# Kernel optimization log

Measured on AMD Instinct MI355X. Metric: run time of the kernel, lower is better.

## Reference

```python
import jax, jax.numpy as jnp
import numpy as np

D_MODEL = 768
N_HEADS = 12
D_FF = 3072
B, T = 1, 4096
EPS = 1e-5


def _linear_params(key, d_in, d_out):
    kw, kb = jax.random.split(key)
    s = 1.0 / np.sqrt(d_in)
    W = jax.random.uniform(kw, (d_in, d_out), jnp.float32, -s, s)
    b = jax.random.uniform(kb, (d_out,), jnp.float32, -s, s)
    return W, b


def setup_inputs() -> dict:
    key = jax.random.key(0)
    keys = jax.random.split(key, 8)
    x = jax.random.normal(keys[0], (B, T, D_MODEL), jnp.float32)
    Wq, bq = _linear_params(keys[1], D_MODEL, D_MODEL)
    Wk, bk = _linear_params(keys[2], D_MODEL, D_MODEL)
    Wv, bv = _linear_params(keys[3], D_MODEL, D_MODEL)
    Wo, bo = _linear_params(keys[4], D_MODEL, D_MODEL)
    W1, b1 = _linear_params(keys[5], D_MODEL, D_FF)
    W2, b2 = _linear_params(keys[6], D_FF, D_MODEL)
    g1 = jnp.ones((D_MODEL,), jnp.float32)
    be1 = jnp.zeros((D_MODEL,), jnp.float32)
    g2 = jnp.ones((D_MODEL,), jnp.float32)
    be2 = jnp.zeros((D_MODEL,), jnp.float32)
    return {"x": x, "Wq": Wq, "bq": bq, "Wk": Wk, "bk": bk, "Wv": Wv, "bv": bv,
            "Wo": Wo, "bo": bo, "W1": W1, "b1": b1, "W2": W2, "b2": b2,
            "g1": g1, "be1": be1, "g2": g2, "be2": be2}


def _layer_norm(x, g, b):
    mu = jnp.mean(x, axis=-1, keepdims=True)
    var = jnp.var(x, axis=-1, keepdims=True)
    return (x - mu) * jax.lax.rsqrt(var + EPS) * g + b


def reference(x, Wq, bq, Wk, bk, Wv, bv, Wo, bo, W1, b1, W2, b2, g1, be1, g2, be2):
    b_, t_, d_ = x.shape
    dk = d_ // N_HEADS
    # QKV projections -> [B, H, T, dk]
    def split_heads(y):
        return y.reshape(b_, t_, N_HEADS, dk).transpose(0, 2, 1, 3)
    q = split_heads(x @ Wq + bq)
    k = split_heads(x @ Wk + bk)
    v = split_heads(x @ Wv + bv)
    # scores [B, H, T, T], causal mask, softmax
    scores = jnp.einsum('bhqd,bhkd->bhqk', q, k) / np.sqrt(dk).astype(np.float32)
    causal = jnp.tril(jnp.ones((t_, t_), dtype=bool))
    scores = jnp.where(causal, scores, -jnp.inf)
    attn = jax.nn.softmax(scores, axis=-1)
    out = jnp.einsum('bhqk,bhkd->bhqd', attn, v)
    out = out.transpose(0, 2, 1, 3).reshape(b_, t_, d_)
    attn_out = out @ Wo + bo
    # residual + LN1
    h = _layer_norm(x + attn_out, g1, be1)
    # FFN
    ff = jax.nn.relu(h @ W1 + b1) @ W2 + b2
    # residual + LN2
    return _layer_norm(h + ff, g2, be2)
```

## Files before the change

### kernel.cpp

```cpp
#include <hip/hip_runtime.h>
#include <math.h>

#define TSEQ 4096
#define DMODEL 768
#define NHEADS 12
#define DKH 64
#define DFF 3072
#define LOG2E 1.44269504f

typedef __attribute__((ext_vector_type(4))) float f32x4;
typedef __attribute__((ext_vector_type(8))) short s16x8;
typedef unsigned short u16;
typedef unsigned int u32;

__device__ __forceinline__ u16 f2bf(float x) {
    u32 u = __builtin_bit_cast(u32, x);
    u32 r = u + 0x7FFFu + ((u >> 16) & 1u);
    return (u16)(r >> 16);
}
__device__ __forceinline__ float bf2f(u16 h) {
    u32 u = ((u32)h) << 16;
    return __builtin_bit_cast(float, u);
}

__device__ __forceinline__ void gll16(const void* g, void* lds) {
    __builtin_amdgcn_global_load_lds(
        (const __attribute__((address_space(1))) u32*)g,
        (__attribute__((address_space(3))) u32*)lds, 16, 0, 0);
}

__global__ __launch_bounds__(256) void tobf16(const float* __restrict__ in,
                                              u16* __restrict__ out, int n4)
{
    int idx = blockIdx.x * 256 + threadIdx.x;
    for (int i = idx; i < n4; i += 262144) {
        float4 v = *(const float4*)(in + (size_t)i * 4);
        *(ushort4*)(out + (size_t)i * 4) =
            make_ushort4(f2bf(v.x), f2bf(v.y), f2bf(v.z), f2bf(v.w));
    }
}

__global__ __launch_bounds__(256) void wtrans4(
    const float* __restrict__ Wq, const float* __restrict__ Wk,
    const float* __restrict__ Wv, const float* __restrict__ Wo,
    u16* __restrict__ Wqkvt, u16* __restrict__ Wot)
{
    __shared__ float t[32 * 33];
    const int z = blockIdx.z;
    const float* W = (z == 0) ? Wq : (z == 1) ? Wk : (z == 2) ? Wv : Wo;
    u16* out = (z < 3) ? Wqkvt : Wot;
    const int nofs = (z < 3) ? z * 768 : 0;
    const int K = 768, N = 768;
    const int tid = threadIdx.x;
    const int kt = blockIdx.y << 5, nt = blockIdx.x << 5;
    const int r = tid >> 3, c4 = tid & 7;
    float4 v = *(const float4*)(W + (size_t)(kt + r) * N + nt + (c4 << 2));
    t[r * 33 + (c4 << 2) + 0] = v.x;
    t[r * 33 + (c4 << 2) + 1] = v.y;
    t[r * 33 + (c4 << 2) + 2] = v.z;
    t[r * 33 + (c4 << 2) + 3] = v.w;
    __syncthreads();
    float a0 = t[((c4 << 2) + 0) * 33 + r];
    float a1 = t[((c4 << 2) + 1) * 33 + r];
    float a2 = t[((c4 << 2) + 2) * 33 + r];
    float a3 = t[((c4 << 2) + 3) * 33 + r];
    u16* o = out + (size_t)(nofs + nt + r) * K + kt + (c4 << 2);
    *(ushort4*)o = make_ushort4(f2bf(a0), f2bf(a1), f2bf(a2), f2bf(a3));
}

__global__ __launch_bounds__(256) void wtrans(const float* __restrict__ W,
                                              u16* __restrict__ out,
                                              int K, int N)
{
    __shared__ float t[32 * 33];
    const int tid = threadIdx.x;
    const int kt = blockIdx.y << 5, nt = blockIdx.x << 5;
    const int r = tid >> 3, c4 = tid & 7;
    float4 v = *(const float4*)(W + (size_t)(kt + r) * N + nt + (c4 << 2));
    t[r * 33 + (c4 << 2) + 0] = v.x;
    t[r * 33 + (c4 << 2) + 1] = v.y;
    t[r * 33 + (c4 << 2) + 2] = v.z;
    t[r * 33 + (c4 << 2) + 3] = v.w;
    __syncthreads();
    float a0 = t[((c4 << 2) + 0) * 33 + r];
    float a1 = t[((c4 << 2) + 1) * 33 + r];
    float a2 = t[((c4 << 2) + 2) * 33 + r];
    float a3 = t[((c4 << 2) + 3) * 33 + r];
    u16* o = out + (size_t)(nt + r) * K + kt + (c4 << 2);
    *(ushort4*)o = make_ushort4(f2bf(a0), f2bf(a1), f2bf(a2), f2bf(a3));
}

__global__ __launch_bounds__(256) void bias_cat_kernel(const float* bq, const float* bk,
                                                       const float* bv, float* o)
{
    int i = blockIdx.x * 256 + threadIdx.x;
    if (i < 768) o[i] = bq[i];
    else if (i < 1536) o[i] = bk[i - 768];
    else if (i < 2304) o[i] = bv[i - 1536];
}

template<int BM, int BN, int EPI>
__global__ __launch_bounds__(256) void gemm_bf(
    const u16* __restrict__ A, const u16* __restrict__ B,
    const float* __restrict__ bias, const float* __restrict__ R,
    float* __restrict__ Cf, u16* __restrict__ Cs,
    u16* __restrict__ Qb, u16* __restrict__ Kb, u16* __restrict__ VTb,
    int N, int KP)
{
    constexpr int FM = BM / 32, FN = BN / 32, NC = BN / 2, NCP = NC + 4;
    __shared__ u16 As[BM * 64];
    __shared__ u16 Bs[BN * 64];
    __shared__ float Ep[4 * 16 * NCP];

    const int tid = threadIdx.x;
    const int w = tid >> 6, lane = tid & 63;
    const int wr = w >> 1, wc = w & 1;
    const int li = lane & 15, g = lane >> 4;

    const int gX = gridDim.x;
    const int nwg = gridDim.x * gridDim.y;
    const int wid = blockIdx.y * gX + blockIdx.x;
    const int qc = nwg >> 3;
    const int nid = (wid & 7) * qc + (wid >> 3);
    const int m0 = (nid / gX) * BM, n0 = (nid % gX) * BN;

    f32x4 acc[FM][FN];
#pragma unroll
    for (int mi = 0; mi < FM; ++mi)
#pragma unroll
        for (int ni = 0; ni < FN; ++ni) acc[mi][ni] = (f32x4){0.f, 0.f, 0.f, 0.f};

    const int row8 = lane >> 3;
    const int cs = (lane & 7) ^ row8;
    const int l7 = li & 7;

    for (int k0 = 0; k0 < KP; k0 += 64) {
        __syncthreads();
#pragma unroll
        for (int i = 0; i < BM / 32; ++i) {
            int inst = w * (BM / 32) + i;
            const u16* gp = A + (size_t)(m0 + inst * 8 + row8) * KP + k0 + cs * 8;
            gll16(gp, &As[inst * 512]);
        }
#pragma unroll
        for (int i = 0; i < BN / 32; ++i) {
            int inst = w * (BN / 32) + i;
            const u16* gp = B + (size_t)(n0 + inst * 8 + row8) * KP + k0 + cs * 8;
            gll16(gp, &Bs[inst * 512]);
        }
        __syncthreads();
        s16x8 af[FM][2], bfr[FN][2];
#pragma unroll
        for (int mi = 0; mi < FM; ++mi) {
            int Ra = wr * (BM / 2) + mi * 16 + li;
#pragma unroll
            for (int dc = 0; dc < 2; ++dc)
                af[mi][dc] = *(const s16x8*)&As[Ra * 64 + ((dc * 4 + g) ^ l7) * 8];
        }
#pragma unroll
        for (int ni = 0; ni < FN; ++ni) {
            int Rb = wc * (BN / 2) + ni * 16 + li;
#pragma unroll
            for (int dc = 0; dc < 2; ++dc)
                bfr[ni][dc] = *(const s16x8*)&Bs[Rb * 64 + ((dc * 4 + g) ^ l7) * 8];
        }
        __builtin_amdgcn_s_setprio(1);
#pragma unroll
        for (int mi = 0; mi < FM; ++mi)
#pragma unroll
            for (int ni = 0; ni < FN; ++ni) {
                acc[mi][ni] = __builtin_amdgcn_mfma_f32_16x16x32_bf16(
                    af[mi][0], bfr[ni][0], acc[mi][ni], 0, 0, 0);
                acc[mi][ni] = __builtin_amdgcn_mfma_f32_16x16x32_bf16(
                    af[mi][1], bfr[ni][1], acc[mi][ni], 0, 0, 0);
            }
        __builtin_amdgcn_s_setprio(0);
    }
    __syncthreads();

    float* ep = Ep + w * 16 * NCP;
    const int colbase = n0 + wc * NC;
    const int rr = lane >> 2, ch = lane & 3;

#pragma unroll
    for (int mi = 0; mi < FM; ++mi) {
#pragma unroll
        for (int ni = 0; ni < FN; ++ni)
#pragma unroll
            for (int r = 0; r < 4; ++r)
                ep[(g * 4 + r) * NCP + ni * 16 + li] = acc[mi][ni][r];
        asm volatile("s_waitcnt lgkmcnt(0)" ::: "memory");

        const int grow0 = m0 + wr * (BM / 2) + mi * 16;
        const int grow = grow0 + rr;

        if constexpr (EPI == 1) {
#pragma unroll
            for (int q = 0; q < NC / 16; ++q) {
                int col = ch * (NC / 4) + q * 4;
                f32x4 v = *(f32x4*)&ep[rr * NCP + col];
                int gn = colbase + col;
                float4 bb = *(const float4*)(bias + gn);
                float4 rv = *(const float4*)(R + (size_t)grow * N + gn);
                float4 ov;
                ov.x = v[0] + bb.x + rv.x; ov.y = v[1] + bb.y + rv.y;
                ov.z = v[2] + bb.z + rv.z; ov.w = v[3] + bb.w + rv.w;
                *(float4*)(Cf + (size_t)grow * N + gn) = ov;
            }
        } else if constexpr (EPI == 2) {
#pragma unroll
            for (int q = 0; q < NC / 16; ++q) {
                int col = ch * (NC / 4) + q * 4;
                f32x4 v = *(f32x4*)&ep[rr * NCP + col];
                int gn = colbase + col;
                float4 bb = *(const float4*)(bias + gn);
                float x0 = fmaxf(v[0] + bb.x, 0.f), x1 = fmaxf(v[1] + bb.y, 0.f);
                float x2 = fmaxf(v[2] + bb.z, 0.f), x3 = fmaxf(v[3] + bb.w, 0.f);
                *(ushort4*)(Cs + (size_t)grow * N + gn) =
                    make_ushort4(f2bf(x0), f2bf(x1), f2bf(x2), f2bf(x3));
            }
        } else {
            const int seg = colbase / 768;
            const int hh = (colbase % 768) >> 6;
            if (seg < 2) {
                u16* dst = (seg == 0) ? Qb : Kb;
                const float sc2 = (seg == 0) ? 0.125f * LOG2E : 1.0f;
#pragma unroll
                for (int q = 0; q < NC / 16; ++q) {
                    int col = ch * (NC / 4) + q * 4;
                    f32x4 v = *(f32x4*)&ep[rr * NCP + col];
                    float4 bb = *(const float4*)(bias + colbase + col);
                    u16 h0 = f2bf((v[0] + bb.x) * sc2);
                    u16 h1 = f2bf((v[1] + bb.y) * sc2);
                    u16 h2 = f2bf((v[2] + bb.z) * sc2);
                    u16 h3 = f2bf((v[3] + bb.w) * sc2);
                    *(ushort4*)&dst[((size_t)(hh << 12) + grow) * 64 + col] =
                        make_ushort4(h0, h1, h2, h3);
                }
            } else {
                float bb = bias[colbase + lane];
                s16x8 pa, pb;
#pragma unroll
                for (int r2 = 0; r2 < 8; ++r2)
                    pa[r2] = (short)f2bf(ep[r2 * NCP + lane] + bb);
#pragma unroll
                for (int r2 = 0; r2 < 8; ++r2)
                    pb[r2] = (short)f2bf(ep[(8 + r2) * NCP + lane] + bb);
                u16* ov = VTb + ((size_t)(hh << 6) + lane) * TSEQ + grow0;
                *(s16x8*)(ov)     = pa;
                *(s16x8*)(ov + 8) = pb;
            }
        }
    }
}

__global__ __launch_bounds__(256) void attn64(
    const u16* __restrict__ Qb, const u16* __restrict__ Kb,
    const u16* __restrict__ VTb, u16* __restrict__ ctxb)
{
    __shared__ u16 Ks[2][4096];
    __shared__ u16 Vs[2][4096];
    __shared__ u16 Ps[4][1024];

    const int tid = threadIdx.x, w = tid >> 6, lane = tid & 63;
    const int g = lane >> 4, li = lane & 15, l7 = lane & 7;
    const int p = blockIdx.x;
    const int h = blockIdx.y;

    const u16* Qh = Qb + ((size_t)h << 18);
    const u16* Kh = Kb + ((size_t)h << 18);
    const u16* Vh = VTb + ((size_t)h << 18);

    const int row8 = lane >> 3;
    const int cs = (lane & 7) ^ row8;

    for (int pass = 0; pass < 2; ++pass) {
        const int qbk = pass ? 63 - p : p;
        const int q0 = qbk << 6;
        const int nkb = qbk + 1;

        s16x8 qf[2];
#pragma unroll
        for (int dc = 0; dc < 2; ++dc)
            qf[dc] = *(const s16x8*)(Qh + (size_t)(q0 + w * 16 + li) * 64 + dc * 32 + g * 8);

        f32x4 o[4];
        float m_ = -1e30f, l_ = 0.f;
#pragma unroll
        for (int d16 = 0; d16 < 4; ++d16) o[d16] = (f32x4){0.f, 0.f, 0.f, 0.f};

#pragma unroll
        for (int i = 0; i < 2; ++i) {
            int inst = w * 2 + i;
            int row = inst * 8 + row8;
            gll16(Kh + (size_t)row * 64 + cs * 8, &Ks[0][inst * 512]);
            gll16(Vh + (size_t)row * TSEQ + cs * 8, &Vs[0][inst * 512]);
        }
        __syncthreads();

        for (int kb = 0; kb < nkb; ++kb) {
            const int cur = kb & 1;
            if (kb + 1 < nkb) {
                const int kn = kb + 1;
#pragma unroll
                for (int i = 0; i < 2; ++i) {
                    int inst = w * 2 + i;
                    int row = inst * 8 + row8;
                    gll16(Kh + (size_t)((kn << 6) + row) * 64 + cs * 8, &Ks[cur ^ 1][inst * 512]);
                    gll16(Vh + (size_t)row * TSEQ + (kn << 6) + cs * 8, &Vs[cur ^ 1][inst * 512]);
                }
            }

            f32x4 s[4];
            __builtin_amdgcn_s_setprio(1);
#pragma unroll
            for (int c = 0; c < 4; ++c) {
                s[c] = (f32x4){0.f, 0.f, 0.f, 0.f};
                s16x8 a0 = *(const s16x8*)&Ks[cur][(c * 16 + li) * 64 + ((g) ^ l7) * 8];
                s16x8 a1 = *(const s16x8*)&Ks[cur][(c * 16 + li) * 64 + ((4 + g) ^ l7) * 8];
                s[c] = __builtin_amdgcn_mfma_f32_16x16x32_bf16(a0, qf[0], s[c], 0, 0, 0);
                s[c] = __builtin_amdgcn_mfma_f32_16x16x32_bf16(a1, qf[1], s[c], 0, 0, 0);
            }
            __builtin_amdgcn_s_setprio(0);

            if (kb == qbk) {
#pragma unroll
                for (int c = 0; c < 4; ++c)
#pragma unroll
                    for (int r = 0; r < 4; ++r) {
                        int kglob = (kb << 6) + c * 16 + g * 4 + r;
                        int qglob = q0 + w * 16 + li;
                        if (kglob > qglob) s[c][r] = -1e30f;
                    }
            }

            float v0 = fmaxf(fmaxf(s[0][0], s[0][1]), fmaxf(s[0][2], s[0][3]));
            float v1 = fmaxf(fmaxf(s[1][0], s[1][1]), fmaxf(s[1][2], s[1][3]));
            float v2 = fmaxf(fmaxf(s[2][0], s[2][1]), fmaxf(s[2][2], s[2][3]));
            float v3 = fmaxf(fmaxf(s[3][0], s[3][1]), fmaxf(s[3][2], s[3][3]));
            float pm = fmaxf(fmaxf(v0, v1), fmaxf(v2, v3));
            pm = fmaxf(pm, __shfl_xor(pm, 16, 64));
            pm = fmaxf(pm, __shfl_xor(pm, 32, 64));

            int ok = (pm <= m_ + 8.f);
            if (!__all(ok)) {
                float mn = fmaxf(m_, pm);
                float sc2 = exp2f(m_ - mn);
                m_ = mn;
                l_ *= sc2;
#pragma unroll
                for (int r = 0; r < 4; ++r) {
                    float os = __shfl(sc2, g * 4 + r, 64);
#pragma unroll
                    for (int d16 = 0; d16 < 4; ++d16) o[d16][r] *= os;
                }
            }

            float rsum = 0.f;
#pragma unroll
            for (int c = 0; c < 4; ++c) {
                float e0 = exp2f(s[c][0] - m_);
                float e1 = exp2f(s[c][1] - m_);
                float e2 = exp2f(s[c][2] - m_);
                float e3 = exp2f(s[c][3] - m_);
                rsum += (e0 + e1) + (e2 + e3);
                *(ushort4*)&Ps[w][li * 64 + ((c * 16 + 4 * g) ^ (l7 << 3))] =
                    make_ushort4(f2bf(e0), f2bf(e1), f2bf(e2), f2bf(e3));
            }
            rsum += __shfl_xor(rsum, 16, 64);
            rsum += __shfl_xor(rsum, 32, 64);
            l_ += rsum;

            asm volatile("s_waitcnt lgkmcnt(0)" ::: "memory");
            __builtin_amdgcn_sched_barrier(0);

            __builtin_amdgcn_s_setprio(1);
#pragma unroll
            for (int ks = 0; ks < 2; ++ks) {
                int koff = ((ks * 4 + g) ^ l7) * 8;
                s16x8 pf = *(const s16x8*)&Ps[w][li * 64 + ((ks * 32 + g * 8) ^ (l7 << 3))];
#pragma unroll
                for (int d16 = 0; d16 < 4; ++d16) {
                    s16x8 vf = *(const s16x8*)&Vs[cur][(d16 * 16 + li) * 64 + koff];
                    o[d16] = __builtin_amdgcn_mfma_f32_16x16x32_bf16(pf, vf, o[d16], 0, 0, 0);
                }
            }
            __builtin_amdgcn_s_setprio(0);
            __syncthreads();
        }

        float il = 1.0f / l_;
#pragma unroll
        for (int r = 0; r < 4; ++r) {
            float iv = __shfl(il, g * 4 + r, 64);
            int qrow = q0 + w * 16 + g * 4 + r;
#pragma unroll
            for (int d16 = 0; d16 < 4; ++d16) {
                int col = (h << 6) + d16 * 16 + li;
                ctxb[(size_t)qrow * DMODEL + col] = f2bf(o[d16][r] * iv);
            }
        }
        __syncthreads();
    }
}

template<int BF>
__global__ __launch_bounds__(256) void ln_kernel(const float* __restrict__ in,
    const float* __restrict__ gw, const float* __restrict__ bw,
    float* __restrict__ outf, u16* __restrict__ outb)
{
    __shared__ float red[8];
    const int row = blockIdx.x, tid = threadIdx.x;
    const float* x = in + (size_t)row * DMODEL;
    float v0 = x[tid], v1 = x[tid + 256], v2 = x[tid + 512];
    float s = v0 + v1 + v2;
#pragma unroll
    for (int off = 32; off > 0; off >>= 1) s += __shfl_xor(s, off, 64);
    const int wv = tid >> 6, lane = tid & 63;
    if (lane == 0) red[wv] = s;
    __syncthreads();
    float mu = (red[0] + red[1] + red[2] + red[3]) * (1.0f / DMODEL);
    float d0 = v0 - mu, d1 = v1 - mu, d2 = v2 - mu;
    float s2 = d0 * d0 + d1 * d1 + d2 * d2;
#pragma unroll
    for (int off = 32; off > 0; off >>= 1) s2 += __shfl_xor(s2, off, 64);
    if (lane == 0) red[4 + wv] = s2;
    __syncthreads();
    float var = (red[4] + red[5] + red[6] + red[7]) * (1.0f / DMODEL);
    float rstd = rsqrtf(var + 1e-5f);
    float y0 = d0 * rstd * gw[tid] + bw[tid];
    float y1 = d1 * rstd * gw[tid + 256] + bw[tid + 256];
    float y2 = d2 * rstd * gw[tid + 512] + bw[tid + 512];
    float* yo = outf + (size_t)row * DMODEL;
    yo[tid] = y0; yo[tid + 256] = y1; yo[tid + 512] = y2;
    if constexpr (BF) {
        u16* o = outb + (size_t)row * DMODEL;
        o[tid] = f2bf(y0); o[tid + 256] = f2bf(y1); o[tid + 512] = f2bf(y2);
    }
}

extern "C" void kernel_launch(void* const* d_in, const int* in_sizes, int n_in,
                              void* d_out, int out_size, void* d_ws, size_t ws_size,
                              hipStream_t stream)
{
    const float* x  = (const float*)d_in[0];
    const float* Wq = (const float*)d_in[1];  const float* bq = (const float*)d_in[2];
    const float* Wk = (const float*)d_in[3];  const float* bk = (const float*)d_in[4];
    const float* Wv = (const float*)d_in[5];  const float* bv = (const float*)d_in[6];
    const float* Wo = (const float*)d_in[7];  const float* bo = (const float*)d_in[8];
    const float* W1 = (const float*)d_in[9];  const float* b1 = (const float*)d_in[10];
    const float* W2 = (const float*)d_in[11]; const float* b2 = (const float*)d_in[12];
    const float* g1 = (const float*)d_in[13]; const float* be1 = (const float*)d_in[14];
    const float* g2 = (const float*)d_in[15]; const float* be2 = (const float*)d_in[16];
    float* out = (float*)d_out;

    char* wsb = (char*)d_ws;
    u16*   xb    = (u16*)(wsb + 0);
    u16*   Wqkvt = (u16*)(wsb + 6291456);
    u16*   Wot   = (u16*)(wsb + 9830400);
    u16*   W1t   = (u16*)(wsb + 11010048);
    u16*   W2t   = (u16*)(wsb + 15728640);
    float* bcat  = (float*)(wsb + 20447232);
    u16*   Qb    = (u16*)(wsb + 20456448);
    u16*   Kb2   = (u16*)(wsb + 26747904);
    u16*   VTb   = (u16*)(wsb + 33039360);
    u16*   ctxb  = (u16*)(wsb + 39330816);
    float* s1    = (float*)(wsb + 45622272);
    float* h     = (float*)(wsb + 58205184);
    u16*   hb    = (u16*)(wsb + 70788096);
    u16*   ff1b  = (u16*)(wsb + 77079552);
    float* t2    = (float*)(wsb + 102245376);

    tobf16<<<1024, 256, 0, stream>>>(x, xb, 786432);
    wtrans4<<<dim3(24, 24, 4), 256, 0, stream>>>(Wq, Wk, Wv, Wo, Wqkvt, Wot);
    wtrans<<<dim3(96, 24), 256, 0, stream>>>(W1, W1t, 768, 3072);
    wtrans<<<dim3(24, 96), 256, 0, stream>>>(W2, W2t, 3072, 768);
    bias_cat_kernel<<<9, 256, 0, stream>>>(bq, bk, bv, bcat);

    gemm_bf<128, 128, 0><<<dim3(18, 32), 256, 0, stream>>>(
        xb, Wqkvt, bcat, nullptr, nullptr, nullptr, Qb, Kb2, VTb, 2304, 768);
    attn64<<<dim3(32, 12), 256, 0, stream>>>(Qb, Kb2, VTb, ctxb);
    gemm_bf<64, 128, 1><<<dim3(6, 64), 256, 0, stream>>>(
        ctxb, Wot, bo, x, s1, nullptr, nullptr, nullptr, nullptr, 768, 768);
    ln_kernel<1><<<4096, 256, 0, stream>>>(s1, g1, be1, h, hb);
    gemm_bf<128, 128, 2><<<dim3(24, 32), 256, 0, stream>>>(
        hb, W1t, b1, nullptr, nullptr, ff1b, nullptr, nullptr, nullptr, 3072, 768);
    gemm_bf<64, 128, 1><<<dim3(6, 64), 256, 0, stream>>>(
        ff1b, W2t, b2, h, t2, nullptr, nullptr, nullptr, nullptr, 768, 3072);
    ln_kernel<0><<<4096, 256, 0, stream>>>(t2, g2, be2, out, nullptr);
}
```

Measured before the change: 386.1 us.

## Tune attention kernel: XCD-aware block remap, deferred row-sum reduction, packed bf16 convert

The attention grid is flattened to 1D, and block IDs are remapped so that consecutive blocks on the same XCD share a head, which should improve L2 reuse of K/V. The per-iteration cross-lane reductions of the row sum are moved to after the loop, and the max reduction now only runs when a rescale is needed. The checks now use per-lane partial maxima. Float-to-bf16 conversion of probabilities uses the hardware v_cvt_pk_bf16_f32 instruction instead of manual rounding. Load address arithmetic is hoisted into base pointers.

```diff
diff --git a/kernel.cpp b/kernel.cpp
--- a/kernel.cpp
+++ b/kernel.cpp
@@ -21,6 +21,11 @@
 __device__ __forceinline__ float bf2f(u16 h) {
     u32 u = ((u32)h) << 16;
     return __builtin_bit_cast(float, u);
+}
+__device__ __forceinline__ u32 cvtpk(float lo, float hi) {
+    u32 r;
+    asm("v_cvt_pk_bf16_f32 %0, %1, %2" : "=v"(r) : "v"(lo), "v"(hi));
+    return r;
 }
 
 __device__ __forceinline__ void gll16(const void* g, void* lds) {
@@ -264,8 +269,10 @@
 
     const int tid = threadIdx.x, w = tid >> 6, lane = tid & 63;
     const int g = lane >> 4, li = lane & 15, l7 = lane & 7;
-    const int p = blockIdx.x;
-    const int h = blockIdx.y;
+    const int wid = blockIdx.x;
+    const int nid = (wid & 7) * 48 + (wid >> 3);
+    const int h = nid >> 5;
+    const int p = nid & 31;
 
     const u16* Qh = Qb + ((size_t)h << 18);
     const u16* Kh = Kb + ((size_t)h << 18);
@@ -284,6 +291,9 @@
         for (int dc = 0; dc < 2; ++dc)
             qf[dc] = *(const s16x8*)(Qh + (size_t)(q0 + w * 16 + li) * 64 + dc * 32 + g * 8);
 
+        const u16* kbase = Kh + (size_t)(w * 16 + row8) * 64 + cs * 8;
+        const u16* vbase = Vh + (size_t)(w * 16 + row8) * TSEQ + cs * 8;
+
         f32x4 o[4];
         float m_ = -1e30f, l_ = 0.f;
 #pragma unroll
@@ -292,9 +302,8 @@
 #pragma unroll
         for (int i = 0; i < 2; ++i) {
             int inst = w * 2 + i;
-            int row = inst * 8 + row8;
-            gll16(Kh + (size_t)row * 64 + cs * 8, &Ks[0][inst * 512]);
-            gll16(Vh + (size_t)row * TSEQ + cs * 8, &Vs[0][inst * 512]);
+            gll16(kbase + (size_t)i * 512, &Ks[0][inst * 512]);
+            gll16(vbase + (size_t)i * 8 * TSEQ, &Vs[0][inst * 512]);
         }
         __syncthreads();
 
@@ -305,9 +314,8 @@
 #pragma unroll
                 for (int i = 0; i < 2; ++i) {
                     int inst = w * 2 + i;
-                    int row = inst * 8 + row8;
-                    gll16(Kh + (size_t)((kn << 6) + row) * 64 + cs * 8, &Ks[cur ^ 1][inst * 512]);
-                    gll16(Vh + (size_t)row * TSEQ + (kn << 6) + cs * 8, &Vs[cur ^ 1][inst * 512]);
+                    gll16(kbase + (size_t)kn * 4096 + (size_t)i * 512, &Ks[cur ^ 1][inst * 512]);
+                    gll16(vbase + (size_t)kn * 64 + (size_t)i * 8 * TSEQ, &Vs[cur ^ 1][inst * 512]);
                 }
             }
 
@@ -338,12 +346,11 @@
             float v1 = fmaxf(fmaxf(s[1][0], s[1][1]), fmaxf(s[1][2], s[1][3]));
             float v2 = fmaxf(fmaxf(s[2][0], s[2][1]), fmaxf(s[2][2], s[2][3]));
             float v3 = fmaxf(fmaxf(s[3][0], s[3][1]), fmaxf(s[3][2], s[3][3]));
-            float pm = fmaxf(fmaxf(v0, v1), fmaxf(v2, v3));
-            pm = fmaxf(pm, __shfl_xor(pm, 16, 64));
-            pm = fmaxf(pm, __shfl_xor(pm, 32, 64));
-
-            int ok = (pm <= m_ + 8.f);
-            if (!__all(ok)) {
+            float pmp = fmaxf(fmaxf(v0, v1), fmaxf(v2, v3));
+
+            if (!__all(pmp <= m_ + 8.f)) {
+                float pm = fmaxf(pmp, __shfl_xor(pmp, 16, 64));
+                pm = fmaxf(pm, __shfl_xor(pm, 32, 64));
                 float mn = fmaxf(m_, pm);
                 float sc2 = exp2f(m_ - mn);
                 m_ = mn;
@@ -356,20 +363,18 @@
                 }
             }
 
-            float rsum = 0.f;
 #pragma unroll
             for (int c = 0; c < 4; ++c) {
                 float e0 = exp2f(s[c][0] - m_);
                 float e1 = exp2f(s[c][1] - m_);
                 float e2 = exp2f(s[c][2] - m_);
                 float e3 = exp2f(s[c][3] - m_);
-                rsum += (e0 + e1) + (e2 + e3);
-                *(ushort4*)&Ps[w][li * 64 + ((c * 16 + 4 * g) ^ (l7 << 3))] =
-                    make_ushort4(f2bf(e0), f2bf(e1), f2bf(e2), f2bf(e3));
-            }
-            rsum += __shfl_xor(rsum, 16, 64);
-            rsum += __shfl_xor(rsum, 32, 64);
-            l_ += rsum;
+                l_ += (e0 + e1) + (e2 + e3);
+                u32 r0 = cvtpk(e0, e1);
+                u32 r1 = cvtpk(e2, e3);
+                *(uint2*)&Ps[w][li * 64 + ((c * 16 + 4 * g) ^ (l7 << 3))] =
+                    make_uint2(r0, r1);
+            }
 
             asm volatile("s_waitcnt lgkmcnt(0)" ::: "memory");
             __builtin_amdgcn_sched_barrier(0);
@@ -389,6 +394,8 @@
             __syncthreads();
         }
 
+        l_ += __shfl_xor(l_, 16, 64);
+        l_ += __shfl_xor(l_, 32, 64);
         float il = 1.0f / l_;
 #pragma unroll
         for (int r = 0; r < 4; ++r) {
@@ -479,7 +486,7 @@
 
     gemm_bf<128, 128, 0><<<dim3(18, 32), 256, 0, stream>>>(
         xb, Wqkvt, bcat, nullptr, nullptr, nullptr, Qb, Kb2, VTb, 2304, 768);
-    attn64<<<dim3(32, 12), 256, 0, stream>>>(Qb, Kb2, VTb, ctxb);
+    attn64<<<384, 256, 0, stream>>>(Qb, Kb2, VTb, ctxb);
     gemm_bf<64, 128, 1><<<dim3(6, 64), 256, 0, stream>>>(
         ctxb, Wot, bo, x, s1, nullptr, nullptr, nullptr, nullptr, 768, 768);
     ln_kernel<1><<<4096, 256, 0, stream>>>(s1, g1, be1, h, hb);
```

New measurement: 372.7 us. -3.5%, faster.
